# Performance work log

Measured on AMD Instinct MI355X. Metric: run time of the kernel, lower is better.

## Reference

```python
import jax, jax.numpy as jnp
import numpy as np

B, N, H, D = 8, 2048, 4, 64  # batch, seq, heads (multi_head_count), head_dim
OUT = 256


def setup_inputs() -> dict:
    key = jax.random.key(0)
    ks = jax.random.split(key, 9)
    s = 0.02
    return {
        "x": jax.random.normal(ks[0], (B, N, H * D), dtype=jnp.float32),
        "Wq": jax.random.normal(ks[1], (H, D, D), dtype=jnp.float32) * s,
        "Wk": jax.random.normal(ks[2], (H, D, D), dtype=jnp.float32) * s,
        "Wv": jax.random.normal(ks[3], (H, D, D), dtype=jnp.float32) * s,
        "bq": jnp.zeros((H, D), dtype=jnp.float32),
        "bk": jnp.zeros((H, D), dtype=jnp.float32),
        "bv": jnp.zeros((H, D), dtype=jnp.float32),
        "Wp": jax.random.normal(ks[4], (H * D, OUT), dtype=jnp.float32) * s,
        "bp": jnp.zeros((OUT,), dtype=jnp.float32),
    }


def reference(x, Wq, Wk, Wv, bq, bk, bv, Wp, bp):
    # x: [b, n, h*d] -> [b, h, n, d]
    b, n, _ = x.shape
    xh = x.reshape(b, n, H, D).transpose(0, 2, 1, 3)
    # per-head Q/K/V with per-head weights (heads selected = [0..H-1], deterministic for num_heads==4)
    q = jnp.einsum("bhnd,hde->bhne", xh, Wq) + bq[None, :, None, :]
    k = jnp.einsum("bhnd,hde->bhne", xh, Wk) + bk[None, :, None, :]
    v = jnp.einsum("bhnd,hde->bhne", xh, Wv) + bv[None, :, None, :]
    scale = 1.0 / jnp.sqrt(jnp.asarray(D, dtype=x.dtype))
    scores = jnp.einsum("bhne,bhme->bhnm", q, k) * scale  # [b,h,n,n]
    attn = jax.nn.softmax(scores, axis=-1)
    o = jnp.einsum("bhnm,bhme->bhne", attn, v)  # [b,h,n,d]
    # concat heads: [b, n, h*d], then final projection
    o = o.transpose(0, 2, 1, 3).reshape(b, n, H * D)
    return o @ Wp + bp
```

## Files before the change

### kernel.cpp

```cpp
#include <hip/hip_runtime.h>

typedef __attribute__((ext_vector_type(4)))  float  f32x4;
typedef __attribute__((ext_vector_type(16))) float  f32x16;
typedef __attribute__((ext_vector_type(8)))  __bf16 bf16x8;
typedef __attribute__((ext_vector_type(2)))  unsigned u32x2;

constexpr int Bv = 8, Nv = 2048, Hv = 4, Dv = 64, OUTv = 256, HD = 256;
constexpr int BH = Bv * Hv;
constexpr size_t PH = (size_t)BH * Nv * Dv;

#if __has_builtin(__builtin_amdgcn_exp2f)
#define EXP2(x) __builtin_amdgcn_exp2f(x)
#else
#define EXP2(x) exp2f(x)
#endif

__device__ __forceinline__ unsigned short f2bf(float f) {
    union { __bf16 h; unsigned short u; } r;
    r.h = (__bf16)f;
    return r.u;
}

__device__ __forceinline__ unsigned pk_bf16(float a, float b) {
    union { __bf16 h[2]; unsigned u; } r;
    r.h[0] = (__bf16)a; r.h[1] = (__bf16)b;
    return r.u;
}

__device__ __forceinline__ uint4 pack8(const float* f) {
    uint4 u;
    u.x = pk_bf16(f[0], f[1]);
    u.y = pk_bf16(f[2], f[3]);
    u.z = pk_bf16(f[4], f[5]);
    u.w = pk_bf16(f[6], f[7]);
    return u;
}

__device__ __forceinline__ void swap32(unsigned a, unsigned b, unsigned& lo, unsigned& hi) {
#if __has_builtin(__builtin_amdgcn_permlane32_swap)
    u32x2 r = __builtin_amdgcn_permlane32_swap(a, b, false, false);
    lo = r.x; hi = r.y;
#else
    const int ishi = (threadIdx.x & 63) >> 5;
    unsigned pa = __shfl_xor(a, 32, 64), pb = __shfl_xor(b, 32, 64);
    lo = ishi ? pb : a;
    hi = ishi ? b : pa;
#endif
}

#define GLOBAL_AS __attribute__((address_space(1)))
#define LDS_AS    __attribute__((address_space(3)))

__global__ __launch_bounds__(256) void wconv_kernel(
    const float* __restrict__ Wq, const float* __restrict__ Wk, const float* __restrict__ Wv,
    const float* __restrict__ Wp,
    unsigned short* __restrict__ Wt3, unsigned short* __restrict__ Wpt)
{
    const int idx = blockIdx.x * 256 + threadIdx.x;
    if (idx < 49152) {
        const int m = idx >> 14, r = idx & 16383;
        const int h = r >> 12, e = (r >> 6) & 63, d = r & 63;
        const float* W = (m == 0) ? Wq : ((m == 1) ? Wk : Wv);
        Wt3[idx] = f2bf(W[(h << 12) + d * 64 + e]);
    } else {
        const int r = idx - 49152;
        const int e = r >> 8, c = r & 255;
        Wpt[r] = f2bf(Wp[c * 256 + e]);
    }
}

__global__ __launch_bounds__(256) void qkv_kernel(
    const float* __restrict__ x,
    const unsigned short* __restrict__ Wt3,
    const float* __restrict__ bq, const float* __restrict__ bk, const float* __restrict__ bv,
    unsigned short* __restrict__ Qb, unsigned short* __restrict__ Kb,
    unsigned short* __restrict__ Vt)
{
    const int h = blockIdx.x & 3;
    const int tt = blockIdx.x >> 2;
    const int tok0 = tt * 64;
    const int t = threadIdx.x, l = t & 63, w = t >> 6;
    const int lg = l >> 4, lc = l & 15;

    __shared__ uint4 Xs[64 * 8];
    __shared__ uint4 Ws[3 * 512];
    __shared__ uint4 Os[64 * 8];

#pragma unroll
    for (int k = 0; k < 6; ++k) {
        const int s = k * 256 + t;
        const int m = s >> 9, sm = s & 511;
        const int e = sm >> 3, cp = sm & 7;
        __builtin_amdgcn_global_load_lds(
            (const GLOBAL_AS unsigned int*)(Wt3 + (m << 14) + (h << 12) + (e << 6) + ((cp ^ (e & 7)) << 3)),
            (LDS_AS unsigned int*)((char*)Ws + (k * 256 + w * 64) * 16),
            16, 0, 0);
    }

    {
        const int r = t >> 2, c4 = t & 3;
        const float* src = x + (size_t)(tok0 + r) * HD + h * Dv + c4 * 16;
        float f[16];
        *(float4*)(f)      = *(const float4*)(src);
        *(float4*)(f + 4)  = *(const float4*)(src + 4);
        *(float4*)(f + 8)  = *(const float4*)(src + 8);
        *(float4*)(f + 12) = *(const float4*)(src + 12);
        Xs[r * 8 + ((c4 * 2)     ^ (r & 7))] = pack8(f);
        Xs[r * 8 + ((c4 * 2 + 1) ^ (r & 7))] = pack8(f + 8);
    }
    asm volatile("s_waitcnt vmcnt(0)" ::: "memory");
    __syncthreads();

    const int ar = w * 16 + lc;
    bf16x8 a[2];
    a[0] = ((const bf16x8*)Xs)[ar * 8 + (lg       ^ (ar & 7))];
    a[1] = ((const bf16x8*)Xs)[ar * 8 + ((4 + lg) ^ (ar & 7))];

    f32x4 acc[3][4];
#pragma unroll
    for (int m = 0; m < 3; ++m)
#pragma unroll
        for (int nt = 0; nt < 4; ++nt) acc[m][nt] = (f32x4){0.f, 0.f, 0.f, 0.f};

#pragma unroll
    for (int kk = 0; kk < 2; ++kk) {
#pragma unroll
        for (int m = 0; m < 3; ++m) {
#pragma unroll
            for (int nt = 0; nt < 4; ++nt) {
                const int br = nt * 16 + lc;
                const bf16x8 b = ((const bf16x8*)Ws)[(m << 9) + br * 8 + ((kk * 4 + lg) ^ (br & 7))];
                acc[m][nt] = __builtin_amdgcn_mfma_f32_16x16x32_bf16(a[kk], b, acc[m][nt], 0, 0, 0);
            }
        }
    }

    const int b_ = tok0 >> 11, n_ = tok0 & (Nv - 1);
    const int bh = b_ * Hv + h;
    unsigned short* Os16 = (unsigned short*)Os;
    const float* biases[3] = {bq + h * Dv, bk + h * Dv, bv + h * Dv};
    const float QSCALE = 0.125f * 1.44269504088896340736f;

#pragma unroll
    for (int m = 0; m < 3; ++m) {
        if (m) __syncthreads();
        if (m < 2) {
#pragma unroll
            for (int nt = 0; nt < 4; ++nt) {
                const int e = nt * 16 + lc;
                const float bias = biases[m][e];
#pragma unroll
                for (int j = 0; j < 4; ++j) {
                    float v = acc[m][nt][j] + bias;
                    if (m == 0) v *= QSCALE;
                    const int row = w * 16 + lg * 4 + j;
                    const int ch = (e >> 3) ^ (row & 7);
                    Os16[row * 64 + ch * 8 + (e & 7)] = f2bf(v);
                }
            }
            __syncthreads();
            const int r = t >> 2, c4 = t & 3;
            unsigned short* dst = (m == 0 ? Qb : Kb) + ((size_t)bh * Nv + n_ + r) * Dv + c4 * 16;
            *(uint4*)dst       = Os[r * 8 + ((c4 * 2)     ^ (r & 7))];
            *(uint4*)(dst + 8) = Os[r * 8 + ((c4 * 2 + 1) ^ (r & 7))];
        } else {
#pragma unroll
            for (int nt = 0; nt < 4; ++nt) {
                const int e = nt * 16 + lc;
                const float bias = biases[2][e];
#pragma unroll
                for (int j = 0; j < 4; ++j) {
                    const int tok = w * 16 + lg * 4 + j;
                    const int ch = (tok >> 3) ^ (e & 7);
                    Os16[e * 64 + ch * 8 + (tok & 7)] = f2bf(acc[2][nt][j] + bias);
                }
            }
            __syncthreads();
            const int e = t >> 2, c4 = t & 3;
            unsigned short* dst = Vt + ((size_t)bh * Dv + e) * Nv + n_ + c4 * 16;
            *(uint4*)dst       = Os[e * 8 + ((c4 * 2)     ^ (e & 7))];
            *(uint4*)(dst + 8) = Os[e * 8 + ((c4 * 2 + 1) ^ (e & 7))];
        }
    }
}

__global__ __launch_bounds__(256, 2) void attn_kernel(
    const unsigned short* __restrict__ Qb, const unsigned short* __restrict__ Kb,
    const unsigned short* __restrict__ Vt, unsigned short* __restrict__ Ob)
{
    const int bh = blockIdx.x & 31;
    const int qt = blockIdx.x >> 5;
    const int t = threadIdx.x, w = t >> 6, l = t & 63;
    const int hi = l >> 5, lc = l & 31;

    __shared__ uint4 Ks[2][128 * 8];
    __shared__ uint4 Vs[2][64 * 16];

    const unsigned short* Kg = Kb + (size_t)bh * Nv * Dv;
    const unsigned short* Vg = Vt + (size_t)bh * Dv * Nv;

    const int q_ = qt * 128 + w * 32 + lc;
    const unsigned short* Qrow = Qb + ((size_t)bh * Nv + q_) * Dv;
    bf16x8 qf[4];
#pragma unroll
    for (int kk = 0; kk < 4; ++kk)
        qf[kk] = *(const bf16x8*)(Qrow + kk * 16 + hi * 8);

    auto stage = [&](int buf, int kt) {
#pragma unroll
        for (int k = 0; k < 4; ++k) {
            const int s = k * 256 + t;
            const int base = k * 256 + w * 64;
            {
                const int r = s >> 3, c = (s & 7) ^ (r & 7);
                __builtin_amdgcn_global_load_lds(
                    (const GLOBAL_AS unsigned int*)(Kg + ((size_t)kt * 128 + r) * Dv + c * 8),
                    (LDS_AS unsigned int*)((char*)&Ks[buf][0] + base * 16),
                    16, 0, 0);
            }
            {
                const int r = s >> 4, c = (s & 15) ^ (r & 15);
                __builtin_amdgcn_global_load_lds(
                    (const GLOBAL_AS unsigned int*)(Vg + (size_t)r * Nv + kt * 128 + c * 8),
                    (LDS_AS unsigned int*)((char*)&Vs[buf][0] + base * 16),
                    16, 0, 0);
            }
        }
    };

    f32x16 o0, o1;
#pragma unroll
    for (int i = 0; i < 16; ++i) { o0[i] = 0.f; o1[i] = 0.f; }
    float m_run = -1e30f, l_part = 0.f;

    stage(0, 0);
    asm volatile("s_waitcnt vmcnt(0)" ::: "memory");
    __syncthreads();

    int cur = 0;
    for (int kt = 0; kt < Nv / 128; ++kt) {
        if (kt < Nv / 128 - 1) stage(cur ^ 1, kt + 1);

        const uint4* KsB = &Ks[cur][0];
        const uint4* VsB = &Vs[cur][0];

        f32x16 s4[4];
#pragma unroll
        for (int nt = 0; nt < 4; ++nt) {
#pragma unroll
            for (int i = 0; i < 16; ++i) s4[nt][i] = 0.f;
        }
        __builtin_amdgcn_s_setprio(1);
#pragma unroll
        for (int kk = 0; kk < 4; ++kk) {
#pragma unroll
            for (int nt = 0; nt < 4; ++nt) {
                const int r = nt * 32 + lc;
                const bf16x8 af = *(const bf16x8*)&KsB[r * 8 + ((kk * 2 + hi) ^ (r & 7))];
                s4[nt] = __builtin_amdgcn_mfma_f32_32x32x16_bf16(af, qf[kk], s4[nt], 0, 0, 0);
            }
        }
        __builtin_amdgcn_s_setprio(0);

        float v16[16];
#pragma unroll
        for (int r = 0; r < 16; ++r)
            v16[r] = fmaxf(fmaxf(s4[0][r], s4[1][r]), fmaxf(s4[2][r], s4[3][r]));
#pragma unroll
        for (int st = 8; st; st >>= 1)
#pragma unroll
            for (int r = 0; r < st; ++r) v16[r] = fmaxf(v16[r], v16[r + st]);
        float tm = fmaxf(v16[0], __shfl_xor(v16[0], 32, 64));

        if (!__all(tm <= m_run + 8.f)) {
            const float m_new = fmaxf(m_run, tm);
            const float sc = EXP2(m_run - m_new);
            m_run = m_new;
            l_part *= sc;
#pragma unroll
            for (int i = 0; i < 16; ++i) { o0[i] *= sc; o1[i] *= sc; }
        }

        float tsa[4] = {0.f, 0.f, 0.f, 0.f};
#pragma unroll
        for (int nt = 0; nt < 4; ++nt) {
#pragma unroll
            for (int r = 0; r < 16; ++r) {
                const float p = EXP2(s4[nt][r] - m_run);
                s4[nt][r] = p;
                tsa[r & 3] += p;
            }
            unsigned c[8];
#pragma unroll
            for (int i = 0; i < 8; ++i) c[i] = pk_bf16(s4[nt][2 * i], s4[nt][2 * i + 1]);

            unsigned d0a, d2a, d1a, d3a, d0b, d2b, d1b, d3b;
            swap32(c[0], c[2], d0a, d2a);
            swap32(c[1], c[3], d1a, d3a);
            swap32(c[4], c[6], d0b, d2b);
            swap32(c[5], c[7], d1b, d3b);

            union { unsigned u[4]; bf16x8 v; } pf0, pf1;
            pf0.u[0] = d0a; pf0.u[1] = d1a; pf0.u[2] = d2a; pf0.u[3] = d3a;
            pf1.u[0] = d0b; pf1.u[1] = d1b; pf1.u[2] = d2b; pf1.u[3] = d3b;

            __builtin_amdgcn_s_setprio(1);
#pragma unroll
            for (int kslow = 0; kslow < 2; ++kslow) {
                const bf16x8 pf = kslow ? pf1.v : pf0.v;
                {
                    const int row = lc;
                    const int ch = (nt * 4 + kslow * 2 + hi) ^ (row & 15);
                    const bf16x8 vf = *(const bf16x8*)&VsB[row * 16 + ch];
                    o0 = __builtin_amdgcn_mfma_f32_32x32x16_bf16(vf, pf, o0, 0, 0, 0);
                }
                {
                    const int row = 32 + lc;
                    const int ch = (nt * 4 + kslow * 2 + hi) ^ (row & 15);
                    const bf16x8 vf = *(const bf16x8*)&VsB[row * 16 + ch];
                    o1 = __builtin_amdgcn_mfma_f32_32x32x16_bf16(vf, pf, o1, 0, 0, 0);
                }
            }
            __builtin_amdgcn_s_setprio(0);
        }
        l_part += (tsa[0] + tsa[1]) + (tsa[2] + tsa[3]);

        if (kt < Nv / 128 - 1) {
            asm volatile("s_waitcnt vmcnt(0)" ::: "memory");
            __syncthreads();
            cur ^= 1;
        }
    }

    const float lf = l_part + __shfl_xor(l_part, 32, 64);
    const float inv = 1.0f / lf;
    const int b_ = bh >> 2, h_ = bh & 3;
    unsigned short* orow = Ob + ((size_t)b_ * Nv + q_) * HD + h_ * Dv;
#pragma unroll
    for (int g = 0; g < 4; ++g) {
        uint2 ua, ub;
        ua.x = pk_bf16(o0[g * 4 + 0] * inv, o0[g * 4 + 1] * inv);
        ua.y = pk_bf16(o0[g * 4 + 2] * inv, o0[g * 4 + 3] * inv);
        ub.x = pk_bf16(o1[g * 4 + 0] * inv, o1[g * 4 + 1] * inv);
        ub.y = pk_bf16(o1[g * 4 + 2] * inv, o1[g * 4 + 3] * inv);
        *(uint2*)(orow + 8 * g + 4 * hi)      = ua;
        *(uint2*)(orow + 32 + 8 * g + 4 * hi) = ub;
    }
}

__global__ __launch_bounds__(256) void proj_kernel(
    const unsigned short* __restrict__ Ob, const unsigned short* __restrict__ Wpt,
    const float* __restrict__ bp, float* __restrict__ out)
{
    const int tok0 = blockIdx.x * 64;
    const int t = threadIdx.x, w = t >> 6, l = t & 63;
    const int hi = l >> 5, lc = l & 31;
    const int tw = w >> 1;

    __shared__ uint4 SH[2560];

    f32x16 acc[4];
#pragma unroll
    for (int ct = 0; ct < 4; ++ct)
#pragma unroll
        for (int i = 0; i < 16; ++i) acc[ct][i] = 0.f;

    for (int kt = 0; kt < 4; ++kt) {
        const int c0 = kt * 64;
        if (kt) __syncthreads();
#pragma unroll
        for (int j = 0; j < 10; ++j) {
            const int s = j * 256 + t;
            const int base = j * 256 + w * 64;
            if (s < 512) {
                const int r = s >> 3, cp = s & 7;
                __builtin_amdgcn_global_load_lds(
                    (const GLOBAL_AS unsigned int*)(Ob + (size_t)(tok0 + r) * HD + c0 + ((cp ^ (r & 7)) << 3)),
                    (LDS_AS unsigned int*)((char*)SH + base * 16),
                    16, 0, 0);
            } else {
                const int sm = s - 512;
                const int e = sm >> 3, cp = sm & 7;
                __builtin_amdgcn_global_load_lds(
                    (const GLOBAL_AS unsigned int*)(Wpt + (size_t)e * HD + c0 + ((cp ^ (e & 7)) << 3)),
                    (LDS_AS unsigned int*)((char*)SH + base * 16),
                    16, 0, 0);
            }
        }
        asm volatile("s_waitcnt vmcnt(0)" ::: "memory");
        __syncthreads();

        const bf16x8* Osh = (const bf16x8*)SH;
        const bf16x8* Wsh = (const bf16x8*)(SH + 512);
        const int r = tw * 32 + lc;
#pragma unroll
        for (int kk = 0; kk < 4; ++kk) {
            const bf16x8 af = Osh[r * 8 + ((kk * 2 + hi) ^ (r & 7))];
#pragma unroll
            for (int ct = 0; ct < 4; ++ct) {
                const int e = (w & 1) * 128 + ct * 32 + lc;
                const bf16x8 bf = Wsh[e * 8 + ((kk * 2 + hi) ^ (e & 7))];
                acc[ct] = __builtin_amdgcn_mfma_f32_32x32x16_bf16(af, bf, acc[ct], 0, 0, 0);
            }
        }
    }

#pragma unroll
    for (int ct = 0; ct < 4; ++ct) {
        const int e = (w & 1) * 128 + ct * 32 + lc;
        const float bias = bp[e];
#pragma unroll
        for (int r = 0; r < 16; ++r) {
            const int tok = tok0 + tw * 32 + (r & 3) + 8 * (r >> 2) + 4 * hi;
            out[(size_t)tok * OUTv + e] = acc[ct][r] + bias;
        }
    }
}

extern "C" void kernel_launch(void* const* d_in, const int* in_sizes, int n_in,
                              void* d_out, int out_size, void* d_ws, size_t ws_size,
                              hipStream_t stream)
{
    const float* x  = (const float*)d_in[0];
    const float* Wq = (const float*)d_in[1];
    const float* Wk = (const float*)d_in[2];
    const float* Wv = (const float*)d_in[3];
    const float* bq = (const float*)d_in[4];
    const float* bk = (const float*)d_in[5];
    const float* bv = (const float*)d_in[6];
    const float* Wp = (const float*)d_in[7];
    const float* bp = (const float*)d_in[8];
    float* out = (float*)d_out;

    unsigned short* us = (unsigned short*)d_ws;
    unsigned short* Qb  = us;
    unsigned short* Kb  = us + PH;
    unsigned short* Vt  = us + 2 * PH;
    unsigned short* Ob  = us + 3 * PH;
    unsigned short* Wt3 = us + 4 * PH;
    unsigned short* Wpt = Wt3 + 49152;

    wconv_kernel<<<448, 256, 0, stream>>>(Wq, Wk, Wv, Wp, Wt3, Wpt);
    qkv_kernel<<<(Bv * Nv / 64) * Hv, 256, 0, stream>>>(x, Wt3, bq, bk, bv, Qb, Kb, Vt);
    attn_kernel<<<(Nv / 128) * BH, 256, 0, stream>>>(Qb, Kb, Vt, Ob);
    proj_kernel<<<Bv * Nv / 64, 256, 0, stream>>>(Ob, Wpt, bp, out);
}
```

Baseline: 154.6 us.

## Shrink attention tiles, compute row sums via MFMA, pre-convert x to bf16

The attention kernel now uses 128-thread blocks with 64 queries and 64-key tiles, which doubles the grid and halves LDS per block. The softmax denominator is accumulated by an extra MFMA against a ones vector instead of scalar adds and a cross-lane shuffle. Input x is converted to bf16 in the weight-conversion kernel, so qkv can load it asynchronously straight into LDS. The trade-off is 50% more MFMA work in the P·V stage, twice as many sync iterations, and an extra global write and read of x in bf16.

```diff
diff --git a/kernel.cpp b/kernel.cpp
--- a/kernel.cpp
+++ b/kernel.cpp
@@ -52,11 +52,21 @@
 #define LDS_AS    __attribute__((address_space(3)))
 
 __global__ __launch_bounds__(256) void wconv_kernel(
+    const float* __restrict__ x,
     const float* __restrict__ Wq, const float* __restrict__ Wk, const float* __restrict__ Wv,
     const float* __restrict__ Wp,
+    unsigned short* __restrict__ Xb,
     unsigned short* __restrict__ Wt3, unsigned short* __restrict__ Wpt)
 {
-    const int idx = blockIdx.x * 256 + threadIdx.x;
+    if (blockIdx.x < 2048) {
+        const size_t g = ((size_t)blockIdx.x * 256 + threadIdx.x) * 8;
+        float f[8];
+        *(float4*)(f)     = *(const float4*)(x + g);
+        *(float4*)(f + 4) = *(const float4*)(x + g + 4);
+        *(uint4*)(Xb + g) = pack8(f);
+        return;
+    }
+    const int idx = (blockIdx.x - 2048) * 256 + threadIdx.x;
     if (idx < 49152) {
         const int m = idx >> 14, r = idx & 16383;
         const int h = r >> 12, e = (r >> 6) & 63, d = r & 63;
@@ -70,7 +80,7 @@
 }
 
 __global__ __launch_bounds__(256) void qkv_kernel(
-    const float* __restrict__ x,
+    const unsigned short* __restrict__ Xb,
     const unsigned short* __restrict__ Wt3,
     const float* __restrict__ bq, const float* __restrict__ bk, const float* __restrict__ bv,
     unsigned short* __restrict__ Qb, unsigned short* __restrict__ Kb,
@@ -87,6 +97,16 @@
     __shared__ uint4 Os[64 * 8];
 
 #pragma unroll
+    for (int k = 0; k < 2; ++k) {
+        const int slot = k * 256 + t;
+        const int r = slot >> 3, cp = slot & 7;
+        const int c = cp ^ (r & 7);
+        __builtin_amdgcn_global_load_lds(
+            (const GLOBAL_AS unsigned int*)(Xb + (size_t)(tok0 + r) * HD + h * Dv + c * 8),
+            (LDS_AS unsigned int*)((char*)Xs + (k * 256 + w * 64) * 16),
+            16, 0, 0);
+    }
+#pragma unroll
     for (int k = 0; k < 6; ++k) {
         const int s = k * 256 + t;
         const int m = s >> 9, sm = s & 511;
@@ -96,18 +116,6 @@
             (LDS_AS unsigned int*)((char*)Ws + (k * 256 + w * 64) * 16),
             16, 0, 0);
     }
-
-    {
-        const int r = t >> 2, c4 = t & 3;
-        const float* src = x + (size_t)(tok0 + r) * HD + h * Dv + c4 * 16;
-        float f[16];
-        *(float4*)(f)      = *(const float4*)(src);
-        *(float4*)(f + 4)  = *(const float4*)(src + 4);
-        *(float4*)(f + 8)  = *(const float4*)(src + 8);
-        *(float4*)(f + 12) = *(const float4*)(src + 12);
-        Xs[r * 8 + ((c4 * 2)     ^ (r & 7))] = pack8(f);
-        Xs[r * 8 + ((c4 * 2 + 1) ^ (r & 7))] = pack8(f + 8);
-    }
     asm volatile("s_waitcnt vmcnt(0)" ::: "memory");
     __syncthreads();
 
@@ -184,7 +192,7 @@
     }
 }
 
-__global__ __launch_bounds__(256, 2) void attn_kernel(
+__global__ __launch_bounds__(128, 2) void attn_kernel(
     const unsigned short* __restrict__ Qb, const unsigned short* __restrict__ Kb,
     const unsigned short* __restrict__ Vt, unsigned short* __restrict__ Ob)
 {
@@ -193,68 +201,71 @@
     const int t = threadIdx.x, w = t >> 6, l = t & 63;
     const int hi = l >> 5, lc = l & 31;
 
-    __shared__ uint4 Ks[2][128 * 8];
-    __shared__ uint4 Vs[2][64 * 16];
+    __shared__ uint4 Ks[2][64 * 8];
+    __shared__ uint4 Vs[2][64 * 8];
 
     const unsigned short* Kg = Kb + (size_t)bh * Nv * Dv;
     const unsigned short* Vg = Vt + (size_t)bh * Dv * Nv;
 
-    const int q_ = qt * 128 + w * 32 + lc;
+    const int q_ = qt * 64 + w * 32 + lc;
     const unsigned short* Qrow = Qb + ((size_t)bh * Nv + q_) * Dv;
     bf16x8 qf[4];
 #pragma unroll
     for (int kk = 0; kk < 4; ++kk)
         qf[kk] = *(const bf16x8*)(Qrow + kk * 16 + hi * 8);
 
+    bf16x8 onesf;
+#pragma unroll
+    for (int i = 0; i < 8; ++i) onesf[i] = (__bf16)1.0f;
+
     auto stage = [&](int buf, int kt) {
 #pragma unroll
-        for (int k = 0; k < 4; ++k) {
-            const int s = k * 256 + t;
-            const int base = k * 256 + w * 64;
-            {
-                const int r = s >> 3, c = (s & 7) ^ (r & 7);
+        for (int k = 0; k < 8; ++k) {
+            const int slot = k * 128 + t;
+            if (k < 4) {
+                const int r = slot >> 3, c = (slot & 7) ^ (r & 7);
                 __builtin_amdgcn_global_load_lds(
-                    (const GLOBAL_AS unsigned int*)(Kg + ((size_t)kt * 128 + r) * Dv + c * 8),
-                    (LDS_AS unsigned int*)((char*)&Ks[buf][0] + base * 16),
+                    (const GLOBAL_AS unsigned int*)(Kg + ((size_t)kt * 64 + r) * Dv + c * 8),
+                    (LDS_AS unsigned int*)((char*)&Ks[buf][0] + (k * 128 + w * 64) * 16),
                     16, 0, 0);
-            }
-            {
-                const int r = s >> 4, c = (s & 15) ^ (r & 15);
+            } else {
+                const int s2 = slot - 512;
+                const int r = s2 >> 3, c = (s2 & 7) ^ (r & 7);
                 __builtin_amdgcn_global_load_lds(
-                    (const GLOBAL_AS unsigned int*)(Vg + (size_t)r * Nv + kt * 128 + c * 8),
-                    (LDS_AS unsigned int*)((char*)&Vs[buf][0] + base * 16),
+                    (const GLOBAL_AS unsigned int*)(Vg + (size_t)r * Nv + kt * 64 + c * 8),
+                    (LDS_AS unsigned int*)((char*)&Vs[buf][0] + ((k - 4) * 128 + w * 64) * 16),
                     16, 0, 0);
             }
         }
     };
 
-    f32x16 o0, o1;
-#pragma unroll
-    for (int i = 0; i < 16; ++i) { o0[i] = 0.f; o1[i] = 0.f; }
-    float m_run = -1e30f, l_part = 0.f;
+    f32x16 o0, o1, o2;
+#pragma unroll
+    for (int i = 0; i < 16; ++i) { o0[i] = 0.f; o1[i] = 0.f; o2[i] = 0.f; }
+    float m_run = -1e30f;
 
     stage(0, 0);
     asm volatile("s_waitcnt vmcnt(0)" ::: "memory");
     __syncthreads();
 
     int cur = 0;
-    for (int kt = 0; kt < Nv / 128; ++kt) {
-        if (kt < Nv / 128 - 1) stage(cur ^ 1, kt + 1);
+    for (int kt = 0; kt < Nv / 64; ++kt) {
+        if (kt < Nv / 64 - 1) stage(cur ^ 1, kt + 1);
 
         const uint4* KsB = &Ks[cur][0];
         const uint4* VsB = &Vs[cur][0];
 
-        f32x16 s4[4];
-#pragma unroll
-        for (int nt = 0; nt < 4; ++nt) {
+        f32x16 s4[2];
+#pragma unroll
+        for (int nt = 0; nt < 2; ++nt)
 #pragma unroll
             for (int i = 0; i < 16; ++i) s4[nt][i] = 0.f;
-        }
+
         __builtin_amdgcn_s_setprio(1);
 #pragma unroll
         for (int kk = 0; kk < 4; ++kk) {
 #pragma unroll
-            for (int nt = 0; nt < 4; ++nt) {
+            for (int nt = 0; nt < 2; ++nt) {
                 const int r = nt * 32 + lc;
                 const bf16x8 af = *(const bf16x8*)&KsB[r * 8 + ((kk * 2 + hi) ^ (r & 7))];
                 s4[nt] = __builtin_amdgcn_mfma_f32_32x32x16_bf16(af, qf[kk], s4[nt], 0, 0, 0);
@@ -264,8 +275,7 @@
 
         float v16[16];
 #pragma unroll
-        for (int r = 0; r < 16; ++r)
-            v16[r] = fmaxf(fmaxf(s4[0][r], s4[1][r]), fmaxf(s4[2][r], s4[3][r]));
+        for (int r = 0; r < 16; ++r) v16[r] = fmaxf(s4[0][r], s4[1][r]);
 #pragma unroll
         for (int st = 8; st; st >>= 1)
 #pragma unroll
@@ -276,20 +286,15 @@
             const float m_new = fmaxf(m_run, tm);
             const float sc = EXP2(m_run - m_new);
             m_run = m_new;
-            l_part *= sc;
-#pragma unroll
-            for (int i = 0; i < 16; ++i) { o0[i] *= sc; o1[i] *= sc; }
-        }
-
-        float tsa[4] = {0.f, 0.f, 0.f, 0.f};
-#pragma unroll
-        for (int nt = 0; nt < 4; ++nt) {
-#pragma unroll
-            for (int r = 0; r < 16; ++r) {
-                const float p = EXP2(s4[nt][r] - m_run);
-                s4[nt][r] = p;
-                tsa[r & 3] += p;
-            }
+#pragma unroll
+            for (int i = 0; i < 16; ++i) { o0[i] *= sc; o1[i] *= sc; o2[i] *= sc; }
+        }
+
+#pragma unroll
+        for (int nt = 0; nt < 2; ++nt) {
+#pragma unroll
+            for (int r = 0; r < 16; ++r) s4[nt][r] = EXP2(s4[nt][r] - m_run);
+
             unsigned c[8];
 #pragma unroll
             for (int i = 0; i < 8; ++i) c[i] = pk_bf16(s4[nt][2 * i], s4[nt][2 * i + 1]);
@@ -308,32 +313,30 @@
 #pragma unroll
             for (int kslow = 0; kslow < 2; ++kslow) {
                 const bf16x8 pf = kslow ? pf1.v : pf0.v;
+                const int ksl = nt * 2 + kslow;
                 {
                     const int row = lc;
-                    const int ch = (nt * 4 + kslow * 2 + hi) ^ (row & 15);
-                    const bf16x8 vf = *(const bf16x8*)&VsB[row * 16 + ch];
+                    const bf16x8 vf = *(const bf16x8*)&VsB[row * 8 + ((ksl * 2 + hi) ^ (row & 7))];
                     o0 = __builtin_amdgcn_mfma_f32_32x32x16_bf16(vf, pf, o0, 0, 0, 0);
                 }
                 {
                     const int row = 32 + lc;
-                    const int ch = (nt * 4 + kslow * 2 + hi) ^ (row & 15);
-                    const bf16x8 vf = *(const bf16x8*)&VsB[row * 16 + ch];
+                    const bf16x8 vf = *(const bf16x8*)&VsB[row * 8 + ((ksl * 2 + hi) ^ (row & 7))];
                     o1 = __builtin_amdgcn_mfma_f32_32x32x16_bf16(vf, pf, o1, 0, 0, 0);
                 }
+                o2 = __builtin_amdgcn_mfma_f32_32x32x16_bf16(onesf, pf, o2, 0, 0, 0);
             }
             __builtin_amdgcn_s_setprio(0);
         }
-        l_part += (tsa[0] + tsa[1]) + (tsa[2] + tsa[3]);
-
-        if (kt < Nv / 128 - 1) {
+
+        if (kt < Nv / 64 - 1) {
             asm volatile("s_waitcnt vmcnt(0)" ::: "memory");
             __syncthreads();
             cur ^= 1;
         }
     }
 
-    const float lf = l_part + __shfl_xor(l_part, 32, 64);
-    const float inv = 1.0f / lf;
+    const float inv = 1.0f / o2[0];
     const int b_ = bh >> 2, h_ = bh & 3;
     unsigned short* orow = Ob + ((size_t)b_ * Nv + q_) * HD + h_ * Dv;
 #pragma unroll
@@ -437,11 +440,12 @@
     unsigned short* Kb  = us + PH;
     unsigned short* Vt  = us + 2 * PH;
     unsigned short* Ob  = us + 3 * PH;
-    unsigned short* Wt3 = us + 4 * PH;
+    unsigned short* Xb  = us + 4 * PH;
+    unsigned short* Wt3 = us + 5 * PH;
     unsigned short* Wpt = Wt3 + 49152;
 
-    wconv_kernel<<<448, 256, 0, stream>>>(Wq, Wk, Wv, Wp, Wt3, Wpt);
-    qkv_kernel<<<(Bv * Nv / 64) * Hv, 256, 0, stream>>>(x, Wt3, bq, bk, bv, Qb, Kb, Vt);
-    attn_kernel<<<(Nv / 128) * BH, 256, 0, stream>>>(Qb, Kb, Vt, Ob);
+    wconv_kernel<<<2048 + 448, 256, 0, stream>>>(x, Wq, Wk, Wv, Wp, Xb, Wt3, Wpt);
+    qkv_kernel<<<(Bv * Nv / 64) * Hv, 256, 0, stream>>>(Xb, Wt3, bq, bk, bv, Qb, Kb, Vt);
+    attn_kernel<<<(Nv / 64) * BH, 128, 0, stream>>>(Qb, Kb, Vt, Ob);
     proj_kernel<<<Bv * Nv / 64, 256, 0, stream>>>(Ob, Wpt, bp, out);
 }
```

Measured after the change: 167.1 us. +8.1%, slower.
